# Performance work log

Hardware: AMD Instinct MI355X
Metric: run time of the kernel (lower is better)

Reference implementation:

```python
import jax, jax.numpy as jnp
import numpy as np

B, T, C = 4, 1024, 1024  # batch, tokens, channel (== head `size`)
H = 8                    # num_heads


def setup_inputs() -> dict:
    key = jax.random.key(0)
    kd, kq, kk, kv = jax.random.split(key, 4)
    data = jax.random.normal(kd, (B, T, C), dtype=jnp.float32)
    # torch nn.Linear(size,size,bias=False) weight is [out,in]; one per head, stacked on axis 0
    s = 1.0 / np.sqrt(C)
    Wq = jax.random.uniform(kq, (H, C, C), dtype=jnp.float32, minval=-s, maxval=s)
    Wk = jax.random.uniform(kk, (H, C, C), dtype=jnp.float32, minval=-s, maxval=s)
    Wv = jax.random.uniform(kv, (H, C, C), dtype=jnp.float32, minval=-s, maxval=s)
    return {"data": data, "Wq": Wq, "Wk": Wk, "Wv": Wv}


def reference(data, Wq, Wk, Wv):
    # per-head projections: y = x @ W.T  -> [B,H,T,C]
    q = jnp.einsum('btc,hdc->bhtd', data, Wq)
    k = jnp.einsum('btc,hdc->bhtd', data, Wk)
    v = jnp.einsum('btc,hdc->bhtd', data, Wv)
    scale = 1.0 / jnp.sqrt(jnp.asarray(C, dtype=data.dtype))
    scores = jnp.einsum('bhtd,bhsd->bhts', q, k) * scale  # [B,H,T,T]
    causal = jnp.tril(jnp.ones((T, T), dtype=bool))
    scores = jnp.where(causal, scores, -jnp.inf)
    w = jax.nn.softmax(scores, axis=-1)
    out = jnp.einsum('bhts,bhsd->bhtd', w, v)            # [B,H,T,C]
    # torch.cat over heads on last dim == [B,T,H,C] reshape to [B,T,H*C]
    return out.transpose(0, 2, 1, 3).reshape(B, T, H * C)
```

## Files before the change

kernel.cpp:

```cpp
#include <hip/hip_runtime.h>
#include <hip/hip_fp16.h>


typedef unsigned short u16;
typedef _Float16 f16x8 __attribute__((ext_vector_type(8)));
typedef float f32x4 __attribute__((ext_vector_type(4)));

__device__ __forceinline__ u16 f2h(float f) {
    union { __half h; u16 u; } cv;
    cv.h = __float2half(f);
    return cv.u;
}
__device__ __forceinline__ float h2f(u16 u) {
    union { __half h; u16 u; } cv;
    cv.u = u;
    return __half2float(cv.h);
}

__device__ __forceinline__ void gload_lds16(const u16* g, const u16* lds_base, unsigned off_bytes) {
    unsigned a32 = (unsigned)(uintptr_t)((const char*)lds_base + off_bytes);
    a32 = __builtin_amdgcn_readfirstlane(a32);
    __builtin_amdgcn_global_load_lds(
        (const __attribute__((address_space(1))) void*)(uintptr_t)g,
        (__attribute__((address_space(3))) void*)a32,
        16, 0, 0);
}

#define M_MT 0
#define M_PROJ 1
#define M_QK 2
#define M_PV 3

template <int MODE>
__global__ __launch_bounds__(512, 2) void mega(
    const u16* __restrict__ dataH, const u16* __restrict__ WvH,
    const u16* __restrict__ WqT, const u16* __restrict__ WkT,
    u16* __restrict__ MTp, u16* __restrict__ Qp, u16* __restrict__ VTa,
    u16* __restrict__ S16, const u16* __restrict__ P16,
    float* __restrict__ outF)
{
    const int C = 1024, T = 1024, HC = 8192;
    const int nb = (MODE == M_MT ? 128 : MODE == M_PROJ ? 1024 :
                    MODE == M_QK ? 320 : 256);
    const int chunk = nb >> 3;
    const int phys = blockIdx.x;
    const int o = (phys & 7) * chunk + (phys >> 3);

    __shared__ u16 lds[8 * 8192];

    const int t = threadIdx.x, w = t >> 6, l = t & 63;
    const int wm = w >> 2, wn = w & 3;
    const int frow = l & 15, fch = l >> 4;
    const int clin = w * 64 + l;
    const int srow = clin >> 2;
    const int sch = (clin & 3) ^ ((clin >> 3) & 3);

    const int NPASS = (MODE == M_PV) ? 2 : 1;

    for (int pass = 0; pass < NPASS; ++pass) {
        const u16 *Ab, *Bb;
        int lda, ldb, ldc, NT, tile_m, tile_n;
        float scale = 1.0f;
        u16* out16 = nullptr;
        float* out32 = nullptr;

        if (MODE == M_MT) {
            const int h = o >> 4, r = o & 15;
            tile_m = r >> 2; tile_n = r & 3;
            Ab = WkT + (size_t)h * C * C + (size_t)tile_m * 256 * C;
            Bb = WqT + (size_t)h * C * C + (size_t)tile_n * 256 * C;
            lda = C; ldb = C; ldc = C;
            out16 = MTp + (size_t)h * C * C;
            NT = 16;
        } else if (MODE == M_PROJ) {
            const int g = o >> 9, r = o & 511;
            if (g == 0) {
                const int s = r >> 6, ww = r & 63;
                tile_n = (s & 3) * 8 + (ww & 7);
                tile_m = (s >> 2) * 8 + (ww >> 3);
                Ab = dataH + (size_t)tile_m * 256 * C;
                Bb = MTp + (size_t)(tile_n >> 2) * C * C + (size_t)(tile_n & 3) * 256 * C;
                lda = C; ldb = C; ldc = HC;
                out16 = Qp;
                NT = 16;
            } else {
                const int vz = r >> 4, rem = r & 15;
                tile_n = rem & 3; tile_m = rem >> 2;
                Ab = WvH + (size_t)(vz & 7) * C * C + (size_t)tile_m * 256 * C;
                Bb = dataH + (size_t)(vz >> 3) * T * C + (size_t)tile_n * 256 * C;
                lda = C; ldb = C; ldc = T;
                out16 = VTa + (size_t)vz * C * T;
                NT = 16;
            }
        } else if (MODE == M_QK) {
            const int qz = o / 10, j = o - qz * 10;
            tile_m = (j >= 1) + (j >= 3) + (j >= 6);
            tile_n = j - (tile_m == 0 ? 0 : tile_m == 1 ? 1 : tile_m == 2 ? 3 : 6);
            Ab = Qp + (size_t)(qz >> 3) * T * HC + (size_t)(qz & 7) * C
                    + (size_t)tile_m * 256 * HC;
            Bb = dataH + (size_t)(qz >> 3) * T * C + (size_t)tile_n * 256 * C;
            lda = HC; ldb = C; ldc = T;
            out16 = S16 + (size_t)qz * T * T;
            scale = 1.0f / 32.0f;
            NT = 16;
        } else {
            const int pz = o >> 3, j = o & 7, x = j & 3, hi = j >> 2;
            tile_m = (pass == 0) ? (hi ? 2 : 3) : (hi ? 1 : 0);
            tile_n = x;
            Ab = P16 + (size_t)pz * T * T + (size_t)tile_m * 256 * T;
            Bb = VTa + (size_t)pz * C * T + (size_t)tile_n * 256 * T;
            lda = T; ldb = T; ldc = HC;
            out32 = outF + (size_t)(pz >> 3) * T * HC + (size_t)(pz & 7) * C;
            NT = (tile_m + 1) * 4;
        }

        const long eA = (long)srow * lda + sch * 8;
        const long eB = (long)srow * ldb + sch * 8;

        f32x4 acc[8][4] = {};
        f16x8 af[4], bf[4];

#define STAGE(DB, MAT, KS, TT) do {                                            \
        const u16* g_ = (MAT == 0 ? Ab + (size_t)(TT) * 64 + (KS) * 32 + eA    \
                                  : Bb + (size_t)(TT) * 64 + (KS) * 32 + eB);  \
        const u16* hb_ = lds + ((((DB) << 2) | ((MAT) << 1) | (KS)) << 13);    \
        gload_lds16(g_, hb_, (unsigned)(w * 64 * 16));                         \
        gload_lds16(g_ + (size_t)128 * (MAT == 0 ? lda : ldb), hb_,            \
                    (unsigned)((512 + w * 64) * 16));                          \
    } while (0)

#define RD(DB, MAT, KS, ROW)                                                   \
    (*(const f16x8*)((const char*)(lds + ((((DB) << 2) | ((MAT) << 1) | (KS)) << 13)) + \
                     ((unsigned)((ROW) * 64 + fch * 16) ^ ((((ROW) >> 1) & 3) << 4))))

#define VM6 do { asm volatile("s_waitcnt vmcnt(6)"); \
                 __builtin_amdgcn_sched_barrier(0); } while (0)
#define VM0 do { asm volatile("s_waitcnt vmcnt(0)"); \
                 __builtin_amdgcn_sched_barrier(0); } while (0)
#define NOPW ((void)0)

#define PH(DB, KS, MH, WAITC, ...) do {                                        \
        if ((MH) == 0) {                                                       \
            _Pragma("unroll") for (int ni = 0; ni < 4; ++ni)                   \
                bf[ni] = RD(DB, 1, KS, wn * 64 + ni * 16 + frow);              \
        }                                                                      \
        _Pragma("unroll") for (int m4 = 0; m4 < 4; ++m4)                       \
            af[m4] = RD(DB, 0, KS, wm * 128 + ((MH) * 4 + m4) * 16 + frow);    \
        __VA_ARGS__;                                                           \
        __builtin_amdgcn_sched_barrier(0);                                     \
        __builtin_amdgcn_s_barrier();                                          \
        asm volatile("s_waitcnt lgkmcnt(0)");                                  \
        __builtin_amdgcn_sched_barrier(0);                                     \
        __builtin_amdgcn_s_setprio(1);                                         \
        _Pragma("unroll") for (int m4 = 0; m4 < 4; ++m4)                       \
            _Pragma("unroll") for (int ni = 0; ni < 4; ++ni)                   \
                acc[(MH) * 4 + m4][ni] = __builtin_amdgcn_mfma_f32_16x16x32_f16( \
                    af[m4], bf[ni], acc[(MH) * 4 + m4][ni], 0, 0, 0);          \
        __builtin_amdgcn_s_setprio(0);                                         \
        __builtin_amdgcn_sched_barrier(0);                                     \
        WAITC;                                                                 \
        __builtin_amdgcn_s_barrier();                                          \
    } while (0)

        STAGE(0, 1, 0, 0); STAGE(0, 0, 0, 0); STAGE(0, 1, 1, 0); STAGE(0, 0, 1, 0);
        STAGE(1, 1, 0, 1); STAGE(1, 0, 0, 1); STAGE(1, 1, 1, 1);
        VM6;
        __builtin_amdgcn_s_barrier();

        for (int tt = 0; tt < NT; tt += 2) {
            const bool more = (tt + 2) < NT;
            PH(0, 0, 0, NOPW, STAGE(1, 0, 1, tt + 1));
            PH(0, 0, 1, NOPW, if (more) STAGE(0, 1, 0, tt + 2));
            PH(0, 1, 0, NOPW, if (more) STAGE(0, 0, 0, tt + 2));
            PH(0, 1, 1, if (more) VM6; else VM0,
                        if (more) STAGE(0, 1, 1, tt + 2));
            PH(1, 0, 0, NOPW, if (more) STAGE(0, 0, 1, tt + 2));
            PH(1, 0, 1, NOPW, if (more) STAGE(1, 1, 0, tt + 3));
            PH(1, 1, 0, NOPW, if (more) STAGE(1, 0, 0, tt + 3));
            PH(1, 1, 1, if (more) VM6; else VM0,
                        if (more) STAGE(1, 1, 1, tt + 3));
        }
#undef PH
#undef RD
#undef STAGE
#undef VM6
#undef VM0
#undef NOPW

        const int r0 = (l >> 4) * 4, cc = l & 15;
#pragma unroll
        for (int mi = 0; mi < 8; ++mi) {
#pragma unroll
            for (int r = 0; r < 4; ++r) {
                size_t grow = (size_t)(tile_m * 256 + wm * 128 + mi * 16 + r0 + r);
#pragma unroll
                for (int ni = 0; ni < 4; ++ni) {
                    int gcol = tile_n * 256 + wn * 64 + ni * 16 + cc;
                    float v = acc[mi][ni][r] * scale;
                    if (MODE == M_PV)
                        out32[grow * ldc + gcol] = v;
                    else
                        out16[grow * ldc + gcol] = f2h(v);
                }
            }
        }
    }
}

__global__ __launch_bounds__(256) void softmax16(
    const u16* __restrict__ S, u16* __restrict__ P)
{
    const int T = 1024;
    const int tq = blockIdx.x, z = blockIdx.y;
    const u16* row = S + ((size_t)z * T + tq) * T;
    u16* prow = P + ((size_t)z * T + tq) * T;
    const int n = tq + 1, tid = threadIdx.x, i0 = tid * 4;
    const int nw = ((tq >> 8) + 1) << 8;

    ushort4 v = ((const ushort4*)row)[tid];
    float e0 = (i0 + 0 < n) ? h2f(v.x) : -1e30f;
    float e1 = (i0 + 1 < n) ? h2f(v.y) : -1e30f;
    float e2 = (i0 + 2 < n) ? h2f(v.z) : -1e30f;
    float e3 = (i0 + 3 < n) ? h2f(v.w) : -1e30f;

    float m = fmaxf(fmaxf(e0, e1), fmaxf(e2, e3));
#pragma unroll
    for (int o = 1; o < 64; o <<= 1) m = fmaxf(m, __shfl_xor(m, o));
    __shared__ float red[4];
    if ((tid & 63) == 0) red[tid >> 6] = m;
    __syncthreads();
    m = fmaxf(fmaxf(red[0], red[1]), fmaxf(red[2], red[3]));

    float p0 = __expf(e0 - m), p1 = __expf(e1 - m);
    float p2 = __expf(e2 - m), p3 = __expf(e3 - m);
    float s = p0 + p1 + p2 + p3;
#pragma unroll
    for (int o = 1; o < 64; o <<= 1) s += __shfl_xor(s, o);
    __shared__ float red2[4];
    if ((tid & 63) == 0) red2[tid >> 6] = s;
    __syncthreads();
    const float inv = 1.0f / (red2[0] + red2[1] + red2[2] + red2[3]);

    if (i0 < nw) {
        ushort4 o4;
        o4.x = f2h(p0 * inv); o4.y = f2h(p1 * inv);
        o4.z = f2h(p2 * inv); o4.w = f2h(p3 * inv);
        ((ushort4*)prow)[tid] = o4;
    }
}

__global__ __launch_bounds__(256) void cast_setup(
    const float* __restrict__ data, const float* __restrict__ Wq,
    const float* __restrict__ Wk, const float* __restrict__ Wv,
    u16* __restrict__ dataH, u16* __restrict__ WqT,
    u16* __restrict__ WkT, u16* __restrict__ WvH)
{
    const int z = blockIdx.z, tx = threadIdx.x, ty = threadIdx.y;
    if (z < 16) {
        const int h = z & 7;
        const float* src = ((z >> 3) ? Wk : Wq) + (size_t)h * 1048576;
        u16* dst = ((z >> 3) ? WkT : WqT) + (size_t)h * 1048576;
        const int r0 = blockIdx.y * 32, c0 = blockIdx.x * 32;
        __shared__ float tile[32][33];
        for (int i = ty; i < 32; i += 8)
            tile[i][tx] = src[(size_t)(r0 + i) * 1024 + c0 + tx];
        __syncthreads();
        for (int i = ty; i < 32; i += 8)
            dst[(size_t)(c0 + i) * 1024 + r0 + tx] = f2h(tile[tx][i]);
    } else {
        const int tid = ty * 32 + tx;
        const int bid = blockIdx.y * 32 + blockIdx.x;
        const int reps = (z == 16) ? 4 : 8;
        const float* src = (z == 16) ? data : Wv;
        u16* dst = (z == 16) ? dataH : WvH;
        for (int k2 = 0; k2 < reps; ++k2) {
            int i = (k2 * 1024 + bid) * 256 + tid;
            float4 v = ((const float4*)src)[i];
            ushort4 o4;
            o4.x = f2h(v.x); o4.y = f2h(v.y); o4.z = f2h(v.z); o4.w = f2h(v.w);
            ((ushort4*)dst)[i] = o4;
        }
    }
}

extern "C" void kernel_launch(void* const* d_in, const int* in_sizes, int n_in,
                              void* d_out, int out_size, void* d_ws, size_t ws_size,
                              hipStream_t stream)
{
    (void)in_sizes; (void)n_in; (void)out_size; (void)ws_size;
    const int B = 4, T = 1024, C = 1024, H = 8;
    const int BT = B * T, HC = H * C;

    const float* data = (const float*)d_in[0];
    const float* Wq = (const float*)d_in[1];
    const float* Wk = (const float*)d_in[2];
    const float* Wv = (const float*)d_in[3];
    float* out = (float*)d_out;

    char* p = (char*)d_ws;
    const size_t nData = (size_t)BT * C;
    const size_t nW = (size_t)H * C * C;
    const size_t nAll = (size_t)BT * HC;
    const size_t nS = (size_t)B * H * T * T;
    u16* dataH = (u16*)p; p += nData * 2;
    u16* WvH = (u16*)p; p += nW * 2;
    u16* WqT = (u16*)p; p += nW * 2;
    u16* WkT = (u16*)p; p += nW * 2;
    u16* MTp = (u16*)p; p += nW * 2;
    u16* Qp = (u16*)p; p += nAll * 2;
    u16* VTa = (u16*)p; p += nAll * 2;
    u16* S16 = (u16*)p; p += nS * 2;
    u16* P16 = (u16*)p; p += nS * 2;

    cast_setup<<<dim3(32, 32, 18), dim3(32, 8), 0, stream>>>(
        data, Wq, Wk, Wv, dataH, WqT, WkT, WvH);

    mega<M_MT><<<dim3(128), dim3(512), 0, stream>>>(
        dataH, WvH, WqT, WkT, MTp, Qp, VTa, S16, P16, out);

    mega<M_PROJ><<<dim3(1024), dim3(512), 0, stream>>>(
        dataH, WvH, WqT, WkT, MTp, Qp, VTa, S16, P16, out);

    mega<M_QK><<<dim3(320), dim3(512), 0, stream>>>(
        dataH, WvH, WqT, WkT, MTp, Qp, VTa, S16, P16, out);

    softmax16<<<dim3(T, B * H), dim3(256), 0, stream>>>(S16, P16);

    mega<M_PV><<<dim3(256), dim3(512), 0, stream>>>(
        dataH, WvH, WqT, WkT, MTp, Qp, VTa, S16, P16, out);
}
```

Baseline: 384.8 us.

## Redistribute V-projection tiles into under-filled MT and QK launches

Moves the 512 V-projection tiles out of the projection launch. 64 go into the MT launch (128 to 192 blocks) and 448 into the QK launch (320 to 768 blocks), so the Q projection launch runs alone with 512 blocks. The aim is to fill idle CUs in the small launches (256 CUs on MI355X) and balance work across the dependent kernel chain. V has no dependency on MT or Q, so this reordering is safe. The cost is that the QK launch becomes heavier and mixes tile types.

```diff
diff --git a/kernel.cpp b/kernel.cpp
--- a/kernel.cpp
+++ b/kernel.cpp
@@ -26,9 +26,9 @@
         16, 0, 0);
 }
 
-#define M_MT 0
-#define M_PROJ 1
-#define M_QK 2
+#define M_A 0
+#define M_B 1
+#define M_C 2
 #define M_PV 3
 
 template <int MODE>
@@ -40,8 +40,8 @@
     float* __restrict__ outF)
 {
     const int C = 1024, T = 1024, HC = 8192;
-    const int nb = (MODE == M_MT ? 128 : MODE == M_PROJ ? 1024 :
-                    MODE == M_QK ? 320 : 256);
+    const int nb = (MODE == M_A ? 192 : MODE == M_B ? 512 :
+                    MODE == M_C ? 768 : 256);
     const int chunk = nb >> 3;
     const int phys = blockIdx.x;
     const int o = (phys & 7) * chunk + (phys >> 3);
@@ -64,7 +64,19 @@
         u16* out16 = nullptr;
         float* out32 = nullptr;
 
-        if (MODE == M_MT) {
+        int vfill = -1;
+        if (MODE == M_A && o >= 128) vfill = o - 128;
+        if (MODE == M_C && o >= 320) vfill = o - 320 + 64;
+
+        if (vfill >= 0) {
+            const int vz = vfill >> 4, rem = vfill & 15;
+            tile_n = rem & 3; tile_m = rem >> 2;
+            Ab = WvH + (size_t)(vz & 7) * C * C + (size_t)tile_m * 256 * C;
+            Bb = dataH + (size_t)(vz >> 3) * T * C + (size_t)tile_n * 256 * C;
+            lda = C; ldb = C; ldc = T;
+            out16 = VTa + (size_t)vz * C * T;
+            NT = 16;
+        } else if (MODE == M_A) {
             const int h = o >> 4, r = o & 15;
             tile_m = r >> 2; tile_n = r & 3;
             Ab = WkT + (size_t)h * C * C + (size_t)tile_m * 256 * C;
@@ -72,27 +84,16 @@
             lda = C; ldb = C; ldc = C;
             out16 = MTp + (size_t)h * C * C;
             NT = 16;
-        } else if (MODE == M_PROJ) {
-            const int g = o >> 9, r = o & 511;
-            if (g == 0) {
-                const int s = r >> 6, ww = r & 63;
-                tile_n = (s & 3) * 8 + (ww & 7);
-                tile_m = (s >> 2) * 8 + (ww >> 3);
-                Ab = dataH + (size_t)tile_m * 256 * C;
-                Bb = MTp + (size_t)(tile_n >> 2) * C * C + (size_t)(tile_n & 3) * 256 * C;
-                lda = C; ldb = C; ldc = HC;
-                out16 = Qp;
-                NT = 16;
-            } else {
-                const int vz = r >> 4, rem = r & 15;
-                tile_n = rem & 3; tile_m = rem >> 2;
-                Ab = WvH + (size_t)(vz & 7) * C * C + (size_t)tile_m * 256 * C;
-                Bb = dataH + (size_t)(vz >> 3) * T * C + (size_t)tile_n * 256 * C;
-                lda = C; ldb = C; ldc = T;
-                out16 = VTa + (size_t)vz * C * T;
-                NT = 16;
-            }
-        } else if (MODE == M_QK) {
+        } else if (MODE == M_B) {
+            const int s = o >> 6, ww = o & 63;
+            tile_n = (s & 3) * 8 + (ww & 7);
+            tile_m = (s >> 2) * 8 + (ww >> 3);
+            Ab = dataH + (size_t)tile_m * 256 * C;
+            Bb = MTp + (size_t)(tile_n >> 2) * C * C + (size_t)(tile_n & 3) * 256 * C;
+            lda = C; ldb = C; ldc = HC;
+            out16 = Qp;
+            NT = 16;
+        } else if (MODE == M_C) {
             const int qz = o / 10, j = o - qz * 10;
             tile_m = (j >= 1) + (j >= 3) + (j >= 6);
             tile_n = j - (tile_m == 0 ? 0 : tile_m == 1 ? 1 : tile_m == 2 ? 3 : 6);
@@ -315,13 +316,13 @@
     cast_setup<<<dim3(32, 32, 18), dim3(32, 8), 0, stream>>>(
         data, Wq, Wk, Wv, dataH, WqT, WkT, WvH);
 
-    mega<M_MT><<<dim3(128), dim3(512), 0, stream>>>(
+    mega<M_A><<<dim3(192), dim3(512), 0, stream>>>(
         dataH, WvH, WqT, WkT, MTp, Qp, VTa, S16, P16, out);
 
-    mega<M_PROJ><<<dim3(1024), dim3(512), 0, stream>>>(
+    mega<M_B><<<dim3(512), dim3(512), 0, stream>>>(
         dataH, WvH, WqT, WkT, MTp, Qp, VTa, S16, P16, out);
 
-    mega<M_QK><<<dim3(320), dim3(512), 0, stream>>>(
+    mega<M_C><<<dim3(768), dim3(512), 0, stream>>>(
         dataH, WvH, WqT, WkT, MTp, Qp, VTa, S16, P16, out);
 
     softmax16<<<dim3(T, B * H), dim3(256), 0, stream>>>(S16, P16);
```

Result: faster. 364.6 us (-5.2%).
